# Kernel tuning notes

Measured on AMD Instinct MI355X. Metric: run time of the kernel, lower is better.

The kernel has to match this reference:

```python
import jax, jax.numpy as jnp
import numpy as np

K = 4      # tagset_size - 2 (real emotion tags)
NT = 6     # tagset_size
START = 4
STOP = 5


def setup_inputs() -> dict:
    key = jax.random.key(0)
    ks = jax.random.split(key, 10)
    B, T = 2048, 2048
    feats = jax.random.normal(ks[0], (B, T, NT), dtype=jnp.float32)
    bias = jax.random.uniform(ks[1], (B, T), dtype=jnp.float32)        # bias_dict values in [0,1)
    tags = jax.random.randint(ks[2], (B, T), 0, K)                     # emotion labels only
    transitions = jax.random.normal(ks[3], (NT, NT), dtype=jnp.float32)
    transitions = transitions.at[START, :].set(-10000.0)
    transitions = transitions.at[:, STOP].set(-10000.0)
    w_shift_in = jax.random.normal(ks[4], (K,), dtype=jnp.float32)
    bias_no = jax.random.normal(ks[5], (1,), dtype=jnp.float32)
    bias_with = jax.random.normal(ks[6], (1,), dtype=jnp.float32)
    w_with_out = jax.random.normal(ks[7], (K,), dtype=jnp.float32)
    w_no_out = jax.random.normal(ks[8], (K,), dtype=jnp.float32)
    multiplier = jax.random.normal(ks[9], (K, K), dtype=jnp.float32)
    multiplier = multiplier.at[jnp.arange(K), jnp.arange(K)].set(-10000.0)
    return dict(feats=feats, bias=bias, tags=tags, transitions=transitions,
                w_shift_in=w_shift_in, bias_no=bias_no, bias_with=bias_with,
                w_with_out=w_with_out, w_no_out=w_no_out, multiplier=multiplier)


def reference(feats, bias, tags, transitions, w_shift_in, bias_no, bias_with,
              w_with_out, w_no_out, multiplier):
    """Batched neg_log_likelihood = forward_alg(feats) - score_sentence(feats, tags)."""
    B, T, _ = feats.shape
    # multiplier_softmax is over dim=0 (columns); diagonal overwritten with -1
    Mmod = jax.nn.softmax(multiplier, axis=0)
    Mmod = Mmod.at[jnp.arange(K), jnp.arange(K)].set(-1.0)

    # per-step transition gate, shape [B,T,K]; branch on bias > 0.5
    b = bias[..., None]
    gates = jnp.where(b > 0.5,
                      w_with_out * jnp.tanh(b * w_shift_in + bias_with),
                      w_no_out * jnp.tanh(b * w_shift_in + bias_no))

    # ---- forward algorithm (log-sum-exp DP over T, vectorized over B) ----
    init = jnp.full((B, NT), -10000.0, dtype=feats.dtype).at[:, START].set(0.0)
    feats_t = jnp.swapaxes(feats, 0, 1)   # [T,B,NT]
    gates_t = jnp.swapaxes(gates, 0, 1)   # [T,B,K]

    def step(alpha, x):
        f, g = x                                          # [B,NT], [B,K]
        blk = g[:, None, :] * Mmod[None, :, :]            # gate[prev] * Mmod[next,prev]
        Teff = transitions[None] + jnp.pad(blk, ((0, 0), (0, 2), (0, 2)))  # [B,NT,NT]
        alpha_new = f + jax.nn.logsumexp(alpha[:, None, :] + Teff, axis=2)
        return alpha_new, None

    alpha, _ = jax.lax.scan(step, init, (feats_t, gates_t))
    fwd_score = jax.nn.logsumexp(alpha + transitions[STOP][None, :], axis=1)  # [B]

    # ---- gold path score ----
    tags_ext = jnp.concatenate(
        [jnp.full((B, 1), START, dtype=tags.dtype), tags], axis=1)
    t0 = tags_ext[:, :-1]   # prev tag, [B,T]
    t1 = tags_ext[:, 1:]    # next tag, [B,T]
    base = transitions[t1, t0]
    Mext = jnp.pad(Mmod, ((0, 2), (0, 2)))
    gate_t0 = jnp.take_along_axis(gates, jnp.clip(t0, 0, K - 1)[..., None], axis=2)[..., 0]
    extra = jnp.where((t0 < K) & (t1 < K), gate_t0 * Mext[t1, t0], 0.0)
    emit = jnp.take_along_axis(feats, t1[..., None], axis=2)[..., 0]
    gold = jnp.sum(base + extra + emit, axis=1) + transitions[STOP, tags[:, -1]]

    return fwd_score - gold  # [B] per-dialog NLL
```

## Files before the change

kernel.cpp:

```cpp
#include <hip/hip_runtime.h>

#define BN 2048
#define TN 2048
#define SLOT 24

__device__ __forceinline__ float ex2(float x){ return __builtin_amdgcn_exp2f(x); }
__device__ __forceinline__ float lg2(float x){ return __builtin_amdgcn_logf(x); }
__device__ __forceinline__ float rcpf(float x){ return __builtin_amdgcn_rcpf(x); }

constexpr float kLog2e = 1.4426950408889634f;
constexpr float kLn2   = 0.6931471805599453f;

__device__ __forceinline__ float fast_tanh(float x){
    float ax = fabsf(x);
    float e  = ex2(ax * (-2.0f * kLog2e));
    float t  = (1.0f - e) * rcpf(1.0f + e);
    return copysignf(t, x);
}

__device__ __forceinline__ float sel4(float v0, float v1, float v2, float v3, int idx){
    float r = (idx == 1) ? v1 : v0;
    r = (idx == 2) ? v2 : r;
    r = (idx == 3) ? v3 : r;
    return r;
}

struct P1Params {
    float AL[4][4], M[4][4];
    float wsv[4], wwv[4], wnv[4];
    float bwc, bnc;
    const float* sA; const float* sM;
    float tc4[4];
};

template <int NCOL>
__device__ __forceinline__ void step_generic(
    const P1Params& pp, float fi0, float fi1, float fi2, float fi3,
    float bv, int tg, bool renorm,
    float (&P)[4][NCOL], float (&lacc)[NCOL], float& gold, int& prev)
{
    const bool hw = bv > 0.5f;
    const float bc = hw ? pp.bwc : pp.bnc;
    float g[4], gL[4];
    #pragma unroll
    for (int j = 0; j < 4; ++j) {
        float x = fmaf(bv, pp.wsv[j], bc);
        g[j]  = (hw ? pp.wwv[j] : pp.wnv[j]) * fast_tanh(x);
        gL[j] = g[j] * kLog2e;
    }
    const float fiL[4] = { fi0 * kLog2e, fi1 * kLog2e, fi2 * kLog2e, fi3 * kLog2e };
    float nP[4][NCOL];
    #pragma unroll
    for (int i = 0; i < 4; ++i)
        #pragma unroll
        for (int j = 0; j < NCOL; ++j) nP[i][j] = 0.0f;
    #pragma unroll
    for (int k = 0; k < 4; ++k) {
        float Ek[4];
        #pragma unroll
        for (int i = 0; i < 4; ++i)
            Ek[i] = ex2(fmaf(gL[k], pp.M[i][k], fiL[i] + pp.AL[i][k]));
        #pragma unroll
        for (int j = 0; j < NCOL; ++j) {
            const float pk = P[k][j];
            #pragma unroll
            for (int i = 0; i < 4; ++i) nP[i][j] = fmaf(Ek[i], pk, nP[i][j]);
        }
    }
    #pragma unroll
    for (int i = 0; i < 4; ++i)
        #pragma unroll
        for (int j = 0; j < NCOL; ++j) P[i][j] = nP[i][j];

    const int idx = tg * 4 + prev;
    gold += pp.sA[idx] + sel4(g[0], g[1], g[2], g[3], prev) * pp.sM[idx]
          + sel4(fi0, fi1, fi2, fi3, tg);
    prev = tg;

    if (renorm) {
        #pragma unroll
        for (int j = 0; j < NCOL; ++j) {
            float m = fmaxf(fmaxf(P[0][j], P[1][j]), fmaxf(P[2][j], P[3][j]));
            int ee = (int)((__float_as_uint(m) >> 23) & 255u) - 126;
            float sc = __uint_as_float((unsigned)(127 - ee) << 23);
            lacc[j] += (float)ee;
            #pragma unroll
            for (int i = 0; i < 4; ++i) P[i][j] *= sc;
        }
    }
}

template <int NCOL, bool C0>
__device__ __forceinline__ void trip4(
    const float4 (&F)[6], const float (&Bv)[4], const int (&Tg)[4],
    const P1Params& pp, float (&P)[4][NCOL], float (&lacc)[NCOL],
    float& gold, int& prev)
{
    #pragma unroll
    for (int p = 0; p < 2; ++p) {
        const float4 fA = F[3*p], fB = F[3*p+1], fC = F[3*p+2];
        {
            const float fi0 = fA.x, fi1 = fA.y, fi2 = fA.z, fi3 = fA.w;
            if (C0 && p == 0) {
                const float a0 = fi0 + pp.tc4[0], a1 = fi1 + pp.tc4[1];
                const float a2 = fi2 + pp.tc4[2], a3 = fi3 + pp.tc4[3];
                const float mx = fmaxf(fmaxf(a0, a1), fmaxf(a2, a3));
                P[0][0] = ex2((a0 - mx) * kLog2e);
                P[1][0] = ex2((a1 - mx) * kLog2e);
                P[2][0] = ex2((a2 - mx) * kLog2e);
                P[3][0] = ex2((a3 - mx) * kLog2e);
                lacc[0] = mx * kLog2e;
                const int tg0 = Tg[0];
                gold = sel4(pp.tc4[0], pp.tc4[1], pp.tc4[2], pp.tc4[3], tg0)
                     + sel4(fi0, fi1, fi2, fi3, tg0);
                prev = tg0;
            } else {
                step_generic<NCOL>(pp, fi0, fi1, fi2, fi3, Bv[2*p], Tg[2*p],
                                   false, P, lacc, gold, prev);
            }
        }
        {
            const float fi0 = fB.z, fi1 = fB.w, fi2 = fC.x, fi3 = fC.y;
            step_generic<NCOL>(pp, fi0, fi1, fi2, fi3, Bv[2*p+1], Tg[2*p+1],
                               (2*p+1) == 3, P, lacc, gold, prev);
        }
    }
}

__global__ void __launch_bounds__(256)
crf_phase1_t(const float* __restrict__ feats, const float* __restrict__ bias,
             const int* __restrict__ tags, const float* __restrict__ trans,
             const float* __restrict__ wsh, const float* __restrict__ bno,
             const float* __restrict__ bwi, const float* __restrict__ wwo,
             const float* __restrict__ wno, const float* __restrict__ mult,
             float* __restrict__ matAll)
{
    const int w = threadIdx.x >> 6;
    const int L = threadIdx.x & 63;
    const int b = blockIdx.x;
    const int c = threadIdx.x;

    __shared__ float4 stage[4 * 384];
    __shared__ float sA[16], sM[16];
    float4* stageW = stage + w * 384;

    if (threadIdx.x < 16) {
        const int i = threadIdx.x >> 2, j = threadIdx.x & 3;
        sA[threadIdx.x] = trans[i * 6 + j];
        const float m0 = mult[j], m1 = mult[4 + j], m2 = mult[8 + j], m3 = mult[12 + j];
        const float mx = fmaxf(fmaxf(m0, m1), fmaxf(m2, m3));
        const float e0 = ex2((m0 - mx) * kLog2e), e1 = ex2((m1 - mx) * kLog2e);
        const float e2 = ex2((m2 - mx) * kLog2e), e3 = ex2((m3 - mx) * kLog2e);
        const float inv = rcpf(e0 + e1 + e2 + e3);
        const float ei = (i == 0) ? e0 : (i == 1) ? e1 : (i == 2) ? e2 : e3;
        sM[threadIdx.x] = (i == j) ? -1.0f : ei * inv;
    }
    __syncthreads();

    P1Params pp;
    #pragma unroll
    for (int i = 0; i < 4; ++i)
        #pragma unroll
        for (int j = 0; j < 4; ++j) {
            pp.AL[i][j] = trans[i * 6 + j] * kLog2e;
            pp.M[i][j]  = sM[i * 4 + j];
        }
    #pragma unroll
    for (int j = 0; j < 4; ++j) { pp.wsv[j] = wsh[j]; pp.wwv[j] = wwo[j]; pp.wnv[j] = wno[j]; }
    pp.bwc = bwi[0]; pp.bnc = bno[0];
    pp.sA = sA; pp.sM = sM;
    pp.tc4[0] = trans[4]; pp.tc4[1] = trans[10]; pp.tc4[2] = trans[16]; pp.tc4[3] = trans[22];

    float BvA[4], BvB[4]; int TgA[4], TgB[4];
    {
        const float4* bp = (const float4*)(bias + (size_t)b * TN + c * 8);
        const float4 b0 = bp[0], b1 = bp[1];
        BvA[0]=b0.x; BvA[1]=b0.y; BvA[2]=b0.z; BvA[3]=b0.w;
        BvB[0]=b1.x; BvB[1]=b1.y; BvB[2]=b1.z; BvB[3]=b1.w;
        const int4* tp = (const int4*)(tags + (size_t)b * TN + c * 8);
        const int4 t0 = tp[0], t1 = tp[1];
        TgA[0]=t0.x; TgA[1]=t0.y; TgA[2]=t0.z; TgA[3]=t0.w;
        TgB[0]=t1.x; TgB[1]=t1.y; TgB[2]=t1.z; TgB[3]=t1.w;
    }
    int prev = 0;
    if (c != 0) prev = tags[(size_t)b * TN + c * 8 - 1];

    const float4* gF = (const float4*)feats + (size_t)b * 3072 + (size_t)w * 768;

    float P1a[4][1], lacc1[1];
    float P4[4][4],  lacc4[4] = {0.f, 0.f, 0.f, 0.f};
    #pragma unroll
    for (int i = 0; i < 4; ++i)
        #pragma unroll
        for (int j = 0; j < 4; ++j) P4[i][j] = (i == j) ? 1.0f : 0.0f;
    float gold = 0.0f;

    #pragma unroll 1
    for (int h = 0; h < 2; ++h) {
        float4 myF[6];
        {
            float4 tF[6];
            const int h6 = h * 6;
            #pragma unroll
            for (int r = 0; r < 6; ++r) {
                const int S  = r * 64 + L;
                const int cS = (S * 10923) >> 16;
                const int j  = S - cS * 6;
                tF[r] = gF[cS * 12 + h6 + j];
            }
            #pragma unroll
            for (int r = 0; r < 6; ++r) {
                const int S  = r * 64 + L;
                const int cS = (S * 10923) >> 16;
                const int j  = S - cS * 6;
                stageW[(j << 6) + ((cS + j) & 63)] = tF[r];
            }
            #pragma unroll
            for (int j = 0; j < 6; ++j)
                myF[j] = stageW[(j << 6) + ((L + j) & 63)];
        }
        if (c == 0) {
            if (h == 0) trip4<1, true >(myF, BvA, TgA, pp, P1a, lacc1, gold, prev);
            else        trip4<1, false>(myF, BvB, TgB, pp, P1a, lacc1, gold, prev);
        } else {
            if (h == 0) trip4<4, false>(myF, BvA, TgA, pp, P4, lacc4, gold, prev);
            else        trip4<4, false>(myF, BvB, TgB, pp, P4, lacc4, gold, prev);
        }
    }

    if (c == 0) {
        #pragma unroll
        for (int i = 0; i < 4; ++i) {
            const float p = P1a[i][0];
            stageW[(i << 6) + ((L + i) & 63)] = make_float4(p, p, p, p);
        }
        stageW[(4 << 6) + ((L + 4) & 63)] = make_float4(lacc1[0], lacc1[0], lacc1[0], lacc1[0]);
        stageW[(5 << 6) + ((L + 5) & 63)] = make_float4(gold, 0.f, 0.f, 0.f);
    } else {
        #pragma unroll
        for (int i = 0; i < 4; ++i)
            stageW[(i << 6) + ((L + i) & 63)] = make_float4(P4[i][0], P4[i][1], P4[i][2], P4[i][3]);
        stageW[(4 << 6) + ((L + 4) & 63)] = make_float4(lacc4[0], lacc4[1], lacc4[2], lacc4[3]);
        stageW[(5 << 6) + ((L + 5) & 63)] = make_float4(gold, 0.f, 0.f, 0.f);
    }
    float4* gout = (float4*)matAll + ((size_t)b * 256 + (size_t)w * 64) * 6;
    #pragma unroll
    for (int r = 0; r < 6; ++r) {
        const int G  = r * 64 + L;
        const int cS = (G * 10923) >> 16;
        const int q  = G - cS * 6;
        gout[G] = stageW[(q << 6) + ((cS + q) & 63)];
    }
}

__device__ __forceinline__ void compose4(
    const float (&Ae)[4][4], const float (&sa)[4],
    const float (&Be)[4][4], const float (&sb)[4],
    float (&Ce)[4][4], float (&sc)[4])
{
    const float maxA = fmaxf(fmaxf(sa[0], sa[1]), fmaxf(sa[2], sa[3]));
    float Ap[4][4];
    #pragma unroll
    for (int k = 0; k < 4; ++k) {
        const float wk = ex2(sa[k] - maxA);
        #pragma unroll
        for (int i = 0; i < 4; ++i) Ap[i][k] = Ae[i][k] * wk;
    }
    #pragma unroll
    for (int j = 0; j < 4; ++j) {
        float c0 = 0.f, c1 = 0.f, c2 = 0.f, c3 = 0.f;
        #pragma unroll
        for (int k = 0; k < 4; ++k) {
            const float bk = Be[k][j];
            c0 = fmaf(Ap[0][k], bk, c0);
            c1 = fmaf(Ap[1][k], bk, c1);
            c2 = fmaf(Ap[2][k], bk, c2);
            c3 = fmaf(Ap[3][k], bk, c3);
        }
        const float m = fmaxf(fmaxf(c0, c1), fmaxf(c2, c3));
        const int ee = (int)((__float_as_uint(m) >> 23) & 255u) - 126;
        const float scf = __uint_as_float((unsigned)(127 - ee) << 23);
        Ce[0][j] = c0 * scf; Ce[1][j] = c1 * scf;
        Ce[2][j] = c2 * scf; Ce[3][j] = c3 * scf;
        sc[j] = sb[j] + maxA + (float)ee;
    }
}

template <int CCv>
__global__ void __launch_bounds__(256)
crf_phase2(const float* __restrict__ matAll, const float* __restrict__ trans,
           const int* __restrict__ tags, float* __restrict__ out)
{
    constexpr int CPL = CCv / 64;
    const int gtid = blockIdx.x * 256 + threadIdx.x;
    const int b = gtid >> 6;
    const int lane = threadIdx.x & 63;

    const float4* base = (const float4*)(matAll + ((size_t)b * CCv + lane * CPL) * SLOT);
    float Pe[4][4], so[4], gold;
    {
        float A[SLOT];
        #pragma unroll
        for (int q = 0; q < SLOT / 4; ++q) {
            const float4 v = base[q];
            A[4*q] = v.x; A[4*q+1] = v.y; A[4*q+2] = v.z; A[4*q+3] = v.w;
        }
        #pragma unroll
        for (int i = 0; i < 4; ++i)
            #pragma unroll
            for (int j = 0; j < 4; ++j) Pe[i][j] = A[i * 4 + j];
        #pragma unroll
        for (int j = 0; j < 4; ++j) so[j] = A[16 + j];
        gold = A[20];
    }
    #pragma unroll
    for (int p = 1; p < CPL; ++p) {
        float A[SLOT];
        #pragma unroll
        for (int q = 0; q < SLOT / 4; ++q) {
            const float4 v = base[p * (SLOT / 4) + q];
            A[4*q] = v.x; A[4*q+1] = v.y; A[4*q+2] = v.z; A[4*q+3] = v.w;
        }
        float Ae[4][4], sa[4];
        #pragma unroll
        for (int i = 0; i < 4; ++i)
            #pragma unroll
            for (int j = 0; j < 4; ++j) Ae[i][j] = A[i * 4 + j];
        #pragma unroll
        for (int j = 0; j < 4; ++j) sa[j] = A[16 + j];
        gold += A[20];
        float Ce[4][4], sc[4];
        compose4(Ae, sa, Pe, so, Ce, sc);
        #pragma unroll
        for (int i = 0; i < 4; ++i)
            #pragma unroll
            for (int j = 0; j < 4; ++j) Pe[i][j] = Ce[i][j];
        #pragma unroll
        for (int j = 0; j < 4; ++j) so[j] = sc[j];
    }

    #pragma unroll
    for (int d = 1; d < 64; d <<= 1) {
        float oP[4][4], os[4];
        #pragma unroll
        for (int i = 0; i < 4; ++i)
            #pragma unroll
            for (int j = 0; j < 4; ++j) oP[i][j] = __shfl_xor(Pe[i][j], d, 64);
        #pragma unroll
        for (int j = 0; j < 4; ++j) os[j] = __shfl_xor(so[j], d, 64);
        const bool hi = (lane & d) != 0;
        float Ae[4][4], Be[4][4], sa[4], sb[4];
        #pragma unroll
        for (int i = 0; i < 4; ++i)
            #pragma unroll
            for (int j = 0; j < 4; ++j) {
                Ae[i][j] = hi ? Pe[i][j] : oP[i][j];
                Be[i][j] = hi ? oP[i][j] : Pe[i][j];
            }
        #pragma unroll
        for (int j = 0; j < 4; ++j) {
            sa[j] = hi ? so[j] : os[j];
            sb[j] = hi ? os[j] : so[j];
        }
        float Ce[4][4], sc[4];
        compose4(Ae, sa, Be, sb, Ce, sc);
        #pragma unroll
        for (int i = 0; i < 4; ++i)
            #pragma unroll
            for (int j = 0; j < 4; ++j) Pe[i][j] = Ce[i][j];
        #pragma unroll
        for (int j = 0; j < 4; ++j) so[j] = sc[j];
    }

    #pragma unroll
    for (int d = 1; d < 64; d <<= 1) gold += __shfl_xor(gold, d, 64);

    if (lane == 0) {
        const float t50 = trans[30], t51 = trans[31], t52 = trans[32], t53 = trans[33];
        const float ssum = Pe[0][0] * ex2(t50 * kLog2e) + Pe[1][0] * ex2(t51 * kLog2e)
                         + Pe[2][0] * ex2(t52 * kLog2e) + Pe[3][0] * ex2(t53 * kLog2e);
        const float fwd = (so[0] + lg2(ssum)) * kLn2;
        const int lastT = tags[(size_t)b * TN + TN - 1];
        const float gfin = gold + sel4(t50, t51, t52, t53, lastT);
        out[b] = fwd - gfin;
    }
}

template <int NCOL, bool CHUNK0, int TCH>
__device__ __forceinline__ void run_chunk_fb(
    int b, int c,
    const float* __restrict__ feats, const float* __restrict__ bias,
    const int* __restrict__ tags, const P1Params& pp,
    float (&P)[4][NCOL], float (&lacc)[NCOL], float& gold, int& prev)
{
    const int t0c = c * TCH;
    #pragma unroll 1
    for (int bt = 0; bt < TCH / 8; ++bt) {
        const int t0 = t0c + bt * 8;
        float Fr[48];
        {
            const float4* fp4 = (const float4*)(feats + ((size_t)b * TN + t0) * 6);
            #pragma unroll
            for (int q = 0; q < 12; ++q) {
                const float4 vv = fp4[q];
                Fr[q*4+0] = vv.x; Fr[q*4+1] = vv.y; Fr[q*4+2] = vv.z; Fr[q*4+3] = vv.w;
            }
        }
        float Bv[8]; int Tg[8];
        {
            const float4* bp4 = (const float4*)(bias + (size_t)b * TN + t0);
            const float4 v0 = bp4[0], v1 = bp4[1];
            Bv[0]=v0.x; Bv[1]=v0.y; Bv[2]=v0.z; Bv[3]=v0.w;
            Bv[4]=v1.x; Bv[5]=v1.y; Bv[6]=v1.z; Bv[7]=v1.w;
            const int4* tp4 = (const int4*)(tags + (size_t)b * TN + t0);
            const int4 u0 = tp4[0], u1 = tp4[1];
            Tg[0]=u0.x; Tg[1]=u0.y; Tg[2]=u0.z; Tg[3]=u0.w;
            Tg[4]=u1.x; Tg[5]=u1.y; Tg[6]=u1.z; Tg[7]=u1.w;
        }
        #pragma unroll
        for (int s = 0; s < 8; ++s) {
            const float fi0 = Fr[s*6+0], fi1 = Fr[s*6+1];
            const float fi2 = Fr[s*6+2], fi3 = Fr[s*6+3];
            if (CHUNK0 && bt == 0 && s == 0) {
                const float a0 = fi0 + pp.tc4[0], a1 = fi1 + pp.tc4[1];
                const float a2 = fi2 + pp.tc4[2], a3 = fi3 + pp.tc4[3];
                const float mx = fmaxf(fmaxf(a0, a1), fmaxf(a2, a3));
                P[0][0] = ex2((a0 - mx) * kLog2e);
                P[1][0] = ex2((a1 - mx) * kLog2e);
                P[2][0] = ex2((a2 - mx) * kLog2e);
                P[3][0] = ex2((a3 - mx) * kLog2e);
                lacc[0] = mx * kLog2e;
                const int tg0 = Tg[0];
                gold = sel4(pp.tc4[0], pp.tc4[1], pp.tc4[2], pp.tc4[3], tg0)
                     + sel4(fi0, fi1, fi2, fi3, tg0);
                prev = tg0;
                continue;
            }
            step_generic<NCOL>(pp, fi0, fi1, fi2, fi3, Bv[s], Tg[s],
                               (s & 3) == 3, P, lacc, gold, prev);
        }
    }
}

template <int CCv>
__global__ void __launch_bounds__(256)
crf_phase1_fb(const float* __restrict__ feats, const float* __restrict__ bias,
              const int* __restrict__ tags, const float* __restrict__ trans,
              const float* __restrict__ wsh, const float* __restrict__ bno,
              const float* __restrict__ bwi, const float* __restrict__ wwo,
              const float* __restrict__ wno, const float* __restrict__ mult,
              float* __restrict__ matAll)
{
    constexpr int TCHv = TN / CCv;
    constexpr int BPB  = 256 / CCv;
    const int b = blockIdx.x * BPB + (threadIdx.x / CCv);
    const int c = threadIdx.x % CCv;

    __shared__ float sA[16], sM[16];
    if (threadIdx.x < 16) {
        const int i = threadIdx.x >> 2, j = threadIdx.x & 3;
        sA[threadIdx.x] = trans[i * 6 + j];
        const float m0 = mult[j], m1 = mult[4 + j], m2 = mult[8 + j], m3 = mult[12 + j];
        const float mx = fmaxf(fmaxf(m0, m1), fmaxf(m2, m3));
        const float e0 = ex2((m0 - mx) * kLog2e), e1 = ex2((m1 - mx) * kLog2e);
        const float e2 = ex2((m2 - mx) * kLog2e), e3 = ex2((m3 - mx) * kLog2e);
        const float inv = rcpf(e0 + e1 + e2 + e3);
        const float ei = (i == 0) ? e0 : (i == 1) ? e1 : (i == 2) ? e2 : e3;
        sM[threadIdx.x] = (i == j) ? -1.0f : ei * inv;
    }
    __syncthreads();

    P1Params pp;
    #pragma unroll
    for (int i = 0; i < 4; ++i)
        #pragma unroll
        for (int j = 0; j < 4; ++j) {
            pp.AL[i][j] = trans[i * 6 + j] * kLog2e;
            pp.M[i][j]  = sM[i * 4 + j];
        }
    #pragma unroll
    for (int j = 0; j < 4; ++j) { pp.wsv[j] = wsh[j]; pp.wwv[j] = wwo[j]; pp.wnv[j] = wno[j]; }
    pp.bwc = bwi[0]; pp.bnc = bno[0];
    pp.sA = sA; pp.sM = sM;
    pp.tc4[0] = trans[4]; pp.tc4[1] = trans[10]; pp.tc4[2] = trans[16]; pp.tc4[3] = trans[22];

    float o[SLOT];
    float gold = 0.0f;
    int prev;
    if (c == 0) {
        float P[4][1], lacc[1];
        run_chunk_fb<1, true, TCHv>(b, 0, feats, bias, tags, pp, P, lacc, gold, prev);
        #pragma unroll
        for (int i = 0; i < 4; ++i)
            #pragma unroll
            for (int j = 0; j < 4; ++j) o[i * 4 + j] = P[i][0];
        #pragma unroll
        for (int j = 0; j < 4; ++j) o[16 + j] = lacc[0];
    } else {
        float P[4][4], lacc[4] = {0.f, 0.f, 0.f, 0.f};
        #pragma unroll
        for (int i = 0; i < 4; ++i)
            #pragma unroll
            for (int j = 0; j < 4; ++j) P[i][j] = (i == j) ? 1.0f : 0.0f;
        prev = tags[(size_t)b * TN + c * TCHv - 1];
        run_chunk_fb<4, false, TCHv>(b, c, feats, bias, tags, pp, P, lacc, gold, prev);
        #pragma unroll
        for (int i = 0; i < 4; ++i)
            #pragma unroll
            for (int j = 0; j < 4; ++j) o[i * 4 + j] = P[i][j];
        #pragma unroll
        for (int j = 0; j < 4; ++j) o[16 + j] = lacc[j];
    }
    o[20] = gold; o[21] = 0.f; o[22] = 0.f; o[23] = 0.f;
    float4* s4 = (float4*)(matAll + ((size_t)b * CCv + c) * SLOT);
    #pragma unroll
    for (int q = 0; q < SLOT / 4; ++q)
        s4[q] = make_float4(o[4*q], o[4*q+1], o[4*q+2], o[4*q+3]);
}

extern "C" void kernel_launch(void* const* d_in, const int* in_sizes, int n_in,
                              void* d_out, int out_size, void* d_ws, size_t ws_size,
                              hipStream_t stream)
{
    const float* feats = (const float*)d_in[0];
    const float* bias  = (const float*)d_in[1];
    const int*   tags  = (const int*)d_in[2];
    const float* trans = (const float*)d_in[3];
    const float* wsh   = (const float*)d_in[4];
    const float* bno   = (const float*)d_in[5];
    const float* bwi   = (const float*)d_in[6];
    const float* wwo   = (const float*)d_in[7];
    const float* wno   = (const float*)d_in[8];
    const float* mult  = (const float*)d_in[9];
    float* out = (float*)d_out;
    float* matAll = (float*)d_ws;

    const size_t need256 = (size_t)BN * 256 * SLOT * sizeof(float);
    const size_t need128 = (size_t)BN * 128 * SLOT * sizeof(float);
    if (ws_size >= need256) {
        crf_phase1_t<<<BN, 256, 0, stream>>>(
            feats, bias, tags, trans, wsh, bno, bwi, wwo, wno, mult, matAll);
        crf_phase2<256><<<(BN * 64) / 256, 256, 0, stream>>>(matAll, trans, tags, out);
    } else if (ws_size >= need128) {
        crf_phase1_fb<128><<<(128 * BN) / 256, 256, 0, stream>>>(
            feats, bias, tags, trans, wsh, bno, bwi, wwo, wno, mult, matAll);
        crf_phase2<128><<<(BN * 64) / 256, 256, 0, stream>>>(matAll, trans, tags, out);
    } else {
        crf_phase1_fb<64><<<(64 * BN) / 256, 256, 0, stream>>>(
            feats, bias, tags, trans, wsh, bno, bwi, wwo, wno, mult, matAll);
        crf_phase2<64><<<(BN * 64) / 256, 256, 0, stream>>>(matAll, trans, tags, out);
    }
}
```

Measured before the change: 227.7 us.

## Fuse chunk-matrix phase and reduction phase into one kernel per sequence

```diff
diff --git a/kernel.cpp b/kernel.cpp
--- a/kernel.cpp
+++ b/kernel.cpp
@@ -2,11 +2,13 @@
 
 #define BN 2048
 #define TN 2048
-#define SLOT 24
 
 __device__ __forceinline__ float ex2(float x){ return __builtin_amdgcn_exp2f(x); }
 __device__ __forceinline__ float lg2(float x){ return __builtin_amdgcn_logf(x); }
 __device__ __forceinline__ float rcpf(float x){ return __builtin_amdgcn_rcpf(x); }
+__device__ __forceinline__ float rfl(float x){
+    return __uint_as_float(__builtin_amdgcn_readfirstlane(__float_as_uint(x)));
+}
 
 constexpr float kLog2e = 1.4426950408889634f;
 constexpr float kLn2   = 0.6931471805599453f;
@@ -127,13 +129,46 @@
     }
 }
 
+__device__ __forceinline__ void compose4(
+    const float (&Ae)[4][4], const float (&sa)[4],
+    const float (&Be)[4][4], const float (&sb)[4],
+    float (&Ce)[4][4], float (&sc)[4])
+{
+    const float maxA = fmaxf(fmaxf(sa[0], sa[1]), fmaxf(sa[2], sa[3]));
+    float Ap[4][4];
+    #pragma unroll
+    for (int k = 0; k < 4; ++k) {
+        const float wk = ex2(sa[k] - maxA);
+        #pragma unroll
+        for (int i = 0; i < 4; ++i) Ap[i][k] = Ae[i][k] * wk;
+    }
+    #pragma unroll
+    for (int j = 0; j < 4; ++j) {
+        float c0 = 0.f, c1 = 0.f, c2 = 0.f, c3 = 0.f;
+        #pragma unroll
+        for (int k = 0; k < 4; ++k) {
+            const float bk = Be[k][j];
+            c0 = fmaf(Ap[0][k], bk, c0);
+            c1 = fmaf(Ap[1][k], bk, c1);
+            c2 = fmaf(Ap[2][k], bk, c2);
+            c3 = fmaf(Ap[3][k], bk, c3);
+        }
+        const float m = fmaxf(fmaxf(c0, c1), fmaxf(c2, c3));
+        const int ee = (int)((__float_as_uint(m) >> 23) & 255u) - 126;
+        const float scf = __uint_as_float((unsigned)(127 - ee) << 23);
+        Ce[0][j] = c0 * scf; Ce[1][j] = c1 * scf;
+        Ce[2][j] = c2 * scf; Ce[3][j] = c3 * scf;
+        sc[j] = sb[j] + maxA + (float)ee;
+    }
+}
+
 __global__ void __launch_bounds__(256)
-crf_phase1_t(const float* __restrict__ feats, const float* __restrict__ bias,
-             const int* __restrict__ tags, const float* __restrict__ trans,
-             const float* __restrict__ wsh, const float* __restrict__ bno,
-             const float* __restrict__ bwi, const float* __restrict__ wwo,
-             const float* __restrict__ wno, const float* __restrict__ mult,
-             float* __restrict__ matAll)
+crf_fused(const float* __restrict__ feats, const float* __restrict__ bias,
+          const int* __restrict__ tags, const float* __restrict__ trans,
+          const float* __restrict__ wsh, const float* __restrict__ bno,
+          const float* __restrict__ bwi, const float* __restrict__ wwo,
+          const float* __restrict__ wno, const float* __restrict__ mult,
+          float* __restrict__ out)
 {
     const int w = threadIdx.x >> 6;
     const int L = threadIdx.x & 63;
@@ -142,6 +177,8 @@
 
     __shared__ float4 stage[4 * 384];
     __shared__ float sA[16], sM[16];
+    __shared__ float red[4][24];
+
     float4* stageW = stage + w * 384;
 
     if (threadIdx.x < 16) {
@@ -162,14 +199,17 @@
     for (int i = 0; i < 4; ++i)
         #pragma unroll
         for (int j = 0; j < 4; ++j) {
-            pp.AL[i][j] = trans[i * 6 + j] * kLog2e;
-            pp.M[i][j]  = sM[i * 4 + j];
-        }
-    #pragma unroll
-    for (int j = 0; j < 4; ++j) { pp.wsv[j] = wsh[j]; pp.wwv[j] = wwo[j]; pp.wnv[j] = wno[j]; }
-    pp.bwc = bwi[0]; pp.bnc = bno[0];
+            pp.AL[i][j] = rfl(trans[i * 6 + j] * kLog2e);
+            pp.M[i][j]  = rfl(sM[i * 4 + j]);
+        }
+    #pragma unroll
+    for (int j = 0; j < 4; ++j) {
+        pp.wsv[j] = rfl(wsh[j]); pp.wwv[j] = rfl(wwo[j]); pp.wnv[j] = rfl(wno[j]);
+    }
+    pp.bwc = rfl(bwi[0]); pp.bnc = rfl(bno[0]);
     pp.sA = sA; pp.sM = sM;
-    pp.tc4[0] = trans[4]; pp.tc4[1] = trans[10]; pp.tc4[2] = trans[16]; pp.tc4[3] = trans[22];
+    pp.tc4[0] = rfl(trans[4]);  pp.tc4[1] = rfl(trans[10]);
+    pp.tc4[2] = rfl(trans[16]); pp.tc4[3] = rfl(trans[22]);
 
     float BvA[4], BvB[4]; int TgA[4], TgB[4];
     {
@@ -228,115 +268,21 @@
         }
     }
 
+    float Pe[4][4], so[4];
     if (c == 0) {
         #pragma unroll
-        for (int i = 0; i < 4; ++i) {
-            const float p = P1a[i][0];
-            stageW[(i << 6) + ((L + i) & 63)] = make_float4(p, p, p, p);
-        }
-        stageW[(4 << 6) + ((L + 4) & 63)] = make_float4(lacc1[0], lacc1[0], lacc1[0], lacc1[0]);
-        stageW[(5 << 6) + ((L + 5) & 63)] = make_float4(gold, 0.f, 0.f, 0.f);
+        for (int i = 0; i < 4; ++i)
+            #pragma unroll
+            for (int j = 0; j < 4; ++j) Pe[i][j] = P1a[i][0];
+        #pragma unroll
+        for (int j = 0; j < 4; ++j) so[j] = lacc1[0];
     } else {
         #pragma unroll
         for (int i = 0; i < 4; ++i)
-            stageW[(i << 6) + ((L + i) & 63)] = make_float4(P4[i][0], P4[i][1], P4[i][2], P4[i][3]);
-        stageW[(4 << 6) + ((L + 4) & 63)] = make_float4(lacc4[0], lacc4[1], lacc4[2], lacc4[3]);
-        stageW[(5 << 6) + ((L + 5) & 63)] = make_float4(gold, 0.f, 0.f, 0.f);
-    }
-    float4* gout = (float4*)matAll + ((size_t)b * 256 + (size_t)w * 64) * 6;
-    #pragma unroll
-    for (int r = 0; r < 6; ++r) {
-        const int G  = r * 64 + L;
-        const int cS = (G * 10923) >> 16;
-        const int q  = G - cS * 6;
-        gout[G] = stageW[(q << 6) + ((cS + q) & 63)];
-    }
-}
-
-__device__ __forceinline__ void compose4(
-    const float (&Ae)[4][4], const float (&sa)[4],
-    const float (&Be)[4][4], const float (&sb)[4],
-    float (&Ce)[4][4], float (&sc)[4])
-{
-    const float maxA = fmaxf(fmaxf(sa[0], sa[1]), fmaxf(sa[2], sa[3]));
-    float Ap[4][4];
-    #pragma unroll
-    for (int k = 0; k < 4; ++k) {
-        const float wk = ex2(sa[k] - maxA);
-        #pragma unroll
-        for (int i = 0; i < 4; ++i) Ap[i][k] = Ae[i][k] * wk;
-    }
-    #pragma unroll
-    for (int j = 0; j < 4; ++j) {
-        float c0 = 0.f, c1 = 0.f, c2 = 0.f, c3 = 0.f;
-        #pragma unroll
-        for (int k = 0; k < 4; ++k) {
-            const float bk = Be[k][j];
-            c0 = fmaf(Ap[0][k], bk, c0);
-            c1 = fmaf(Ap[1][k], bk, c1);
-            c2 = fmaf(Ap[2][k], bk, c2);
-            c3 = fmaf(Ap[3][k], bk, c3);
-        }
-        const float m = fmaxf(fmaxf(c0, c1), fmaxf(c2, c3));
-        const int ee = (int)((__float_as_uint(m) >> 23) & 255u) - 126;
-        const float scf = __uint_as_float((unsigned)(127 - ee) << 23);
-        Ce[0][j] = c0 * scf; Ce[1][j] = c1 * scf;
-        Ce[2][j] = c2 * scf; Ce[3][j] = c3 * scf;
-        sc[j] = sb[j] + maxA + (float)ee;
-    }
-}
-
-template <int CCv>
-__global__ void __launch_bounds__(256)
-crf_phase2(const float* __restrict__ matAll, const float* __restrict__ trans,
-           const int* __restrict__ tags, float* __restrict__ out)
-{
-    constexpr int CPL = CCv / 64;
-    const int gtid = blockIdx.x * 256 + threadIdx.x;
-    const int b = gtid >> 6;
-    const int lane = threadIdx.x & 63;
-
-    const float4* base = (const float4*)(matAll + ((size_t)b * CCv + lane * CPL) * SLOT);
-    float Pe[4][4], so[4], gold;
-    {
-        float A[SLOT];
-        #pragma unroll
-        for (int q = 0; q < SLOT / 4; ++q) {
-            const float4 v = base[q];
-            A[4*q] = v.x; A[4*q+1] = v.y; A[4*q+2] = v.z; A[4*q+3] = v.w;
-        }
-        #pragma unroll
-        for (int i = 0; i < 4; ++i)
-            #pragma unroll
-            for (int j = 0; j < 4; ++j) Pe[i][j] = A[i * 4 + j];
-        #pragma unroll
-        for (int j = 0; j < 4; ++j) so[j] = A[16 + j];
-        gold = A[20];
-    }
-    #pragma unroll
-    for (int p = 1; p < CPL; ++p) {
-        float A[SLOT];
-        #pragma unroll
-        for (int q = 0; q < SLOT / 4; ++q) {
-            const float4 v = base[p * (SLOT / 4) + q];
-            A[4*q] = v.x; A[4*q+1] = v.y; A[4*q+2] = v.z; A[4*q+3] = v.w;
-        }
-        float Ae[4][4], sa[4];
-        #pragma unroll
-        for (int i = 0; i < 4; ++i)
-            #pragma unroll
-            for (int j = 0; j < 4; ++j) Ae[i][j] = A[i * 4 + j];
-        #pragma unroll
-        for (int j = 0; j < 4; ++j) sa[j] = A[16 + j];
-        gold += A[20];
-        float Ce[4][4], sc[4];
-        compose4(Ae, sa, Pe, so, Ce, sc);
-        #pragma unroll
-        for (int i = 0; i < 4; ++i)
-            #pragma unroll
-            for (int j = 0; j < 4; ++j) Pe[i][j] = Ce[i][j];
-        #pragma unroll
-        for (int j = 0; j < 4; ++j) so[j] = sc[j];
+            #pragma unroll
+            for (int j = 0; j < 4; ++j) Pe[i][j] = P4[i][j];
+        #pragma unroll
+        for (int j = 0; j < 4; ++j) so[j] = lacc4[j];
     }
 
     #pragma unroll
@@ -348,7 +294,7 @@
             for (int j = 0; j < 4; ++j) oP[i][j] = __shfl_xor(Pe[i][j], d, 64);
         #pragma unroll
         for (int j = 0; j < 4; ++j) os[j] = __shfl_xor(so[j], d, 64);
-        const bool hi = (lane & d) != 0;
+        const bool hi = (L & d) != 0;
         float Ae[4][4], Be[4][4], sa[4], sb[4];
         #pragma unroll
         for (int i = 0; i < 4; ++i)
@@ -371,151 +317,53 @@
         #pragma unroll
         for (int j = 0; j < 4; ++j) so[j] = sc[j];
     }
-
     #pragma unroll
     for (int d = 1; d < 64; d <<= 1) gold += __shfl_xor(gold, d, 64);
 
-    if (lane == 0) {
+    if (L == 0) {
+        #pragma unroll
+        for (int i = 0; i < 4; ++i)
+            #pragma unroll
+            for (int j = 0; j < 4; ++j) red[w][i * 4 + j] = Pe[i][j];
+        #pragma unroll
+        for (int j = 0; j < 4; ++j) red[w][16 + j] = so[j];
+        red[w][20] = gold;
+    }
+    __syncthreads();
+    if (threadIdx.x == 0) {
+        float Pt[4][4], st[4];
+        #pragma unroll
+        for (int i = 0; i < 4; ++i)
+            #pragma unroll
+            for (int j = 0; j < 4; ++j) Pt[i][j] = red[0][i * 4 + j];
+        #pragma unroll
+        for (int j = 0; j < 4; ++j) st[j] = red[0][16 + j];
+        float gsum = red[0][20] + red[1][20] + red[2][20] + red[3][20];
+        #pragma unroll
+        for (int ww = 1; ww < 4; ++ww) {
+            float Ae[4][4], sa[4], Ce[4][4], scv[4];
+            #pragma unroll
+            for (int i = 0; i < 4; ++i)
+                #pragma unroll
+                for (int j = 0; j < 4; ++j) Ae[i][j] = red[ww][i * 4 + j];
+            #pragma unroll
+            for (int j = 0; j < 4; ++j) sa[j] = red[ww][16 + j];
+            compose4(Ae, sa, Pt, st, Ce, scv);
+            #pragma unroll
+            for (int i = 0; i < 4; ++i)
+                #pragma unroll
+                for (int j = 0; j < 4; ++j) Pt[i][j] = Ce[i][j];
+            #pragma unroll
+            for (int j = 0; j < 4; ++j) st[j] = scv[j];
+        }
         const float t50 = trans[30], t51 = trans[31], t52 = trans[32], t53 = trans[33];
-        const float ssum = Pe[0][0] * ex2(t50 * kLog2e) + Pe[1][0] * ex2(t51 * kLog2e)
-                         + Pe[2][0] * ex2(t52 * kLog2e) + Pe[3][0] * ex2(t53 * kLog2e);
-        const float fwd = (so[0] + lg2(ssum)) * kLn2;
+        const float ssum = Pt[0][0] * ex2(t50 * kLog2e) + Pt[1][0] * ex2(t51 * kLog2e)
+                         + Pt[2][0] * ex2(t52 * kLog2e) + Pt[3][0] * ex2(t53 * kLog2e);
+        const float fwd = (st[0] + lg2(ssum)) * kLn2;
         const int lastT = tags[(size_t)b * TN + TN - 1];
-        const float gfin = gold + sel4(t50, t51, t52, t53, lastT);
+        const float gfin = gsum + sel4(t50, t51, t52, t53, lastT);
         out[b] = fwd - gfin;
     }
-}
-
-template <int NCOL, bool CHUNK0, int TCH>
-__device__ __forceinline__ void run_chunk_fb(
-    int b, int c,
-    const float* __restrict__ feats, const float* __restrict__ bias,
-    const int* __restrict__ tags, const P1Params& pp,
-    float (&P)[4][NCOL], float (&lacc)[NCOL], float& gold, int& prev)
-{
-    const int t0c = c * TCH;
-    #pragma unroll 1
-    for (int bt = 0; bt < TCH / 8; ++bt) {
-        const int t0 = t0c + bt * 8;
-        float Fr[48];
-        {
-            const float4* fp4 = (const float4*)(feats + ((size_t)b * TN + t0) * 6);
-            #pragma unroll
-            for (int q = 0; q < 12; ++q) {
-                const float4 vv = fp4[q];
-                Fr[q*4+0] = vv.x; Fr[q*4+1] = vv.y; Fr[q*4+2] = vv.z; Fr[q*4+3] = vv.w;
-            }
-        }
-        float Bv[8]; int Tg[8];
-        {
-            const float4* bp4 = (const float4*)(bias + (size_t)b * TN + t0);
-            const float4 v0 = bp4[0], v1 = bp4[1];
-            Bv[0]=v0.x; Bv[1]=v0.y; Bv[2]=v0.z; Bv[3]=v0.w;
-            Bv[4]=v1.x; Bv[5]=v1.y; Bv[6]=v1.z; Bv[7]=v1.w;
-            const int4* tp4 = (const int4*)(tags + (size_t)b * TN + t0);
-            const int4 u0 = tp4[0], u1 = tp4[1];
-            Tg[0]=u0.x; Tg[1]=u0.y; Tg[2]=u0.z; Tg[3]=u0.w;
-            Tg[4]=u1.x; Tg[5]=u1.y; Tg[6]=u1.z; Tg[7]=u1.w;
-        }
-        #pragma unroll
-        for (int s = 0; s < 8; ++s) {
-            const float fi0 = Fr[s*6+0], fi1 = Fr[s*6+1];
-            const float fi2 = Fr[s*6+2], fi3 = Fr[s*6+3];
-            if (CHUNK0 && bt == 0 && s == 0) {
-                const float a0 = fi0 + pp.tc4[0], a1 = fi1 + pp.tc4[1];
-                const float a2 = fi2 + pp.tc4[2], a3 = fi3 + pp.tc4[3];
-                const float mx = fmaxf(fmaxf(a0, a1), fmaxf(a2, a3));
-                P[0][0] = ex2((a0 - mx) * kLog2e);
-                P[1][0] = ex2((a1 - mx) * kLog2e);
-                P[2][0] = ex2((a2 - mx) * kLog2e);
-                P[3][0] = ex2((a3 - mx) * kLog2e);
-                lacc[0] = mx * kLog2e;
-                const int tg0 = Tg[0];
-                gold = sel4(pp.tc4[0], pp.tc4[1], pp.tc4[2], pp.tc4[3], tg0)
-                     + sel4(fi0, fi1, fi2, fi3, tg0);
-                prev = tg0;
-                continue;
-            }
-            step_generic<NCOL>(pp, fi0, fi1, fi2, fi3, Bv[s], Tg[s],
-                               (s & 3) == 3, P, lacc, gold, prev);
-        }
-    }
-}
-
-template <int CCv>
-__global__ void __launch_bounds__(256)
-crf_phase1_fb(const float* __restrict__ feats, const float* __restrict__ bias,
-              const int* __restrict__ tags, const float* __restrict__ trans,
-              const float* __restrict__ wsh, const float* __restrict__ bno,
-              const float* __restrict__ bwi, const float* __restrict__ wwo,
-              const float* __restrict__ wno, const float* __restrict__ mult,
-              float* __restrict__ matAll)
-{
-    constexpr int TCHv = TN / CCv;
-    constexpr int BPB  = 256 / CCv;
-    const int b = blockIdx.x * BPB + (threadIdx.x / CCv);
-    const int c = threadIdx.x % CCv;
-
-    __shared__ float sA[16], sM[16];
-    if (threadIdx.x < 16) {
-        const int i = threadIdx.x >> 2, j = threadIdx.x & 3;
-        sA[threadIdx.x] = trans[i * 6 + j];
-        const float m0 = mult[j], m1 = mult[4 + j], m2 = mult[8 + j], m3 = mult[12 + j];
-        const float mx = fmaxf(fmaxf(m0, m1), fmaxf(m2, m3));
-        const float e0 = ex2((m0 - mx) * kLog2e), e1 = ex2((m1 - mx) * kLog2e);
-        const float e2 = ex2((m2 - mx) * kLog2e), e3 = ex2((m3 - mx) * kLog2e);
-        const float inv = rcpf(e0 + e1 + e2 + e3);
-        const float ei = (i == 0) ? e0 : (i == 1) ? e1 : (i == 2) ? e2 : e3;
-        sM[threadIdx.x] = (i == j) ? -1.0f : ei * inv;
-    }
-    __syncthreads();
-
-    P1Params pp;
-    #pragma unroll
-    for (int i = 0; i < 4; ++i)
-        #pragma unroll
-        for (int j = 0; j < 4; ++j) {
-            pp.AL[i][j] = trans[i * 6 + j] * kLog2e;
-            pp.M[i][j]  = sM[i * 4 + j];
-        }
-    #pragma unroll
-    for (int j = 0; j < 4; ++j) { pp.wsv[j] = wsh[j]; pp.wwv[j] = wwo[j]; pp.wnv[j] = wno[j]; }
-    pp.bwc = bwi[0]; pp.bnc = bno[0];
-    pp.sA = sA; pp.sM = sM;
-    pp.tc4[0] = trans[4]; pp.tc4[1] = trans[10]; pp.tc4[2] = trans[16]; pp.tc4[3] = trans[22];
-
-    float o[SLOT];
-    float gold = 0.0f;
-    int prev;
-    if (c == 0) {
-        float P[4][1], lacc[1];
-        run_chunk_fb<1, true, TCHv>(b, 0, feats, bias, tags, pp, P, lacc, gold, prev);
-        #pragma unroll
-        for (int i = 0; i < 4; ++i)
-            #pragma unroll
-            for (int j = 0; j < 4; ++j) o[i * 4 + j] = P[i][0];
-        #pragma unroll
-        for (int j = 0; j < 4; ++j) o[16 + j] = lacc[0];
-    } else {
-        float P[4][4], lacc[4] = {0.f, 0.f, 0.f, 0.f};
-        #pragma unroll
-        for (int i = 0; i < 4; ++i)
-            #pragma unroll
-            for (int j = 0; j < 4; ++j) P[i][j] = (i == j) ? 1.0f : 0.0f;
-        prev = tags[(size_t)b * TN + c * TCHv - 1];
-        run_chunk_fb<4, false, TCHv>(b, c, feats, bias, tags, pp, P, lacc, gold, prev);
-        #pragma unroll
-        for (int i = 0; i < 4; ++i)
-            #pragma unroll
-            for (int j = 0; j < 4; ++j) o[i * 4 + j] = P[i][j];
-        #pragma unroll
-        for (int j = 0; j < 4; ++j) o[16 + j] = lacc[j];
-    }
-    o[20] = gold; o[21] = 0.f; o[22] = 0.f; o[23] = 0.f;
-    float4* s4 = (float4*)(matAll + ((size_t)b * CCv + c) * SLOT);
-    #pragma unroll
-    for (int q = 0; q < SLOT / 4; ++q)
-        s4[q] = make_float4(o[4*q], o[4*q+1], o[4*q+2], o[4*q+3]);
 }
 
 extern "C" void kernel_launch(void* const* d_in, const int* in_sizes, int n_in,
@@ -533,21 +381,8 @@
     const float* wno   = (const float*)d_in[8];
     const float* mult  = (const float*)d_in[9];
     float* out = (float*)d_out;
-    float* matAll = (float*)d_ws;
-
-    const size_t need256 = (size_t)BN * 256 * SLOT * sizeof(float);
-    const size_t need128 = (size_t)BN * 128 * SLOT * sizeof(float);
-    if (ws_size >= need256) {
-        crf_phase1_t<<<BN, 256, 0, stream>>>(
-            feats, bias, tags, trans, wsh, bno, bwi, wwo, wno, mult, matAll);
-        crf_phase2<256><<<(BN * 64) / 256, 256, 0, stream>>>(matAll, trans, tags, out);
-    } else if (ws_size >= need128) {
-        crf_phase1_fb<128><<<(128 * BN) / 256, 256, 0, stream>>>(
-            feats, bias, tags, trans, wsh, bno, bwi, wwo, wno, mult, matAll);
-        crf_phase2<128><<<(BN * 64) / 256, 256, 0, stream>>>(matAll, trans, tags, out);
-    } else {
-        crf_phase1_fb<64><<<(64 * BN) / 256, 256, 0, stream>>>(
-            feats, bias, tags, trans, wsh, bno, bwi, wwo, wno, mult, matAll);
-        crf_phase2<64><<<(BN * 64) / 256, 256, 0, stream>>>(matAll, trans, tags, out);
-    }
-}
+    (void)d_ws; (void)ws_size;
+
+    crf_fused<<<BN, 256, 0, stream>>>(
+        feats, bias, tags, trans, wsh, bno, bwi, wwo, wno, mult, out);
+}
```

New measurement: 236.4 us. 1.04x slower.
